# Kernel tuning notes

Hardware: AMD Instinct MI355X
Metric: run time of the kernel (lower is better)

## Reference

```python
import jax, jax.numpy as jnp
import numpy as np

INPUT_DIM = 10
SIG_DEPTH = 3
HIDDEN = 64
D_AUG = INPUT_DIM + 1  # time augmentation
LOGSIG_DIM = min(sum(D_AUG ** k // max(1, k) for k in range(1, SIG_DEPTH + 1)), 512)  # = 512
B, N = 1024, 256


def _compute_logsigs(features):
    """Vectorized computation of the per-step prefix-path signature features.

    For prefix length k+1 the torch code time-augments with linspace(0,1,k+1),
    i.e. dt = 1/k, which makes the time-related signature terms k-dependent.
    All terms reduce to cumulative sums over t, computed once for all k.
    Returns (B, N, LOGSIG_DIM); row k=0 is zeros (torch uses zeros at k=0).
    """
    Bsz, n, D = features.shape
    d = D + 1  # augmented dim (time first)
    dtype = features.dtype
    x0 = features[:, :1, :]
    inc = features[:, 1:, :] - features[:, :-1, :]          # (B, n-1, D) feature increments
    rel = features - x0                                      # x_t - x_0, (B, n, D)
    t_idx = jnp.arange(n - 1, dtype=dtype)
    # A[k-1] = sum_{t<k} t * dx_t   (time-row of level-2 term, before dt scaling)
    A = jnp.cumsum(t_idx[None, :, None] * inc, axis=1)       # (B, n-1, D)
    # Bc[k-1] = sum_{t=0}^{k-1} (x_t - x_0)   (time-column, before dt scaling)
    Bc = jnp.cumsum(rel[:, :-1, :], axis=1)                  # (B, n-1, D)
    # C[k-1] = sum_{t<k} (x_t - x_0) outer dx_t  (feature-feature level-2 block)
    C = jnp.cumsum(rel[:, :-1, :, None] * inc[:, :, None, :], axis=1)  # (B, n-1, D, D)
    ks = jnp.arange(1, n, dtype=dtype)                       # k = 1..n-1
    inv_k = 1.0 / ks
    tt = 0.5 * (ks - 1) * inv_k                              # sum t*dt^2 = (k-1)/(2k)
    # level-1: [T=1, x_k - x_0]
    sig1 = jnp.concatenate([jnp.ones((Bsz, n - 1, 1), dtype), rel[:, 1:, :]], axis=-1)  # (B, n-1, d)
    # level-2 matrix, augmented order [time, features]
    sig2 = jnp.zeros((Bsz, n - 1, d, d), dtype)
    sig2 = sig2.at[:, :, 0, 0].set(tt[None, :])
    sig2 = sig2.at[:, :, 0, 1:].set(inv_k[None, :, None] * A)
    sig2 = sig2.at[:, :, 1:, 0].set(inv_k[None, :, None] * Bc)
    sig2 = sig2.at[:, :, 1:, 1:].set(C)
    sig2f = sig2.reshape(Bsz, n - 1, d * d)
    # level-3 (torch: flatten(sig1 outer sig2_flat), truncated); only build needed rows
    sig3_len = LOGSIG_DIM - d - d * d                        # 512 - 11 - 121 = 380
    rows = (sig3_len + d * d - 1) // (d * d)                 # 4 rows of sig1 suffice
    sig3 = (sig1[..., :rows, None] * sig2f[..., None, :]).reshape(Bsz, n - 1, rows * d * d)[..., :sig3_len]
    logsig = jnp.concatenate([sig1, sig2f, sig3], axis=-1)[..., :LOGSIG_DIM]  # (B, n-1, 512)
    return jnp.concatenate([jnp.zeros((Bsz, 1, LOGSIG_DIM), dtype), logsig], axis=1)


def setup_inputs() -> dict:
    key = jax.random.key(0)
    k0, k1, k2, k3 = jax.random.split(key, 4)
    features = jax.random.normal(k0, (B, N, INPUT_DIM), jnp.float32)
    in_dim = LOGSIG_DIM + INPUT_DIM + 1  # 523
    W1 = jax.random.normal(k1, (in_dim, HIDDEN), jnp.float32) / np.sqrt(in_dim)
    b1 = jnp.zeros((HIDDEN,), jnp.float32)
    W2 = jax.random.normal(k2, (HIDDEN, HIDDEN), jnp.float32) / np.sqrt(HIDDEN)
    b2 = jnp.zeros((HIDDEN,), jnp.float32)
    W3 = jax.random.normal(k3, (HIDDEN, 1), jnp.float32) / np.sqrt(HIDDEN)
    b3 = jnp.zeros((1,), jnp.float32)
    return {"features": features, "W1": W1, "b1": b1, "W2": W2, "b2": b2, "W3": W3, "b3": b3}


def reference(features, W1, b1, W2, b2, W3, b3):
    logsigs = _compute_logsigs(features)  # (B, N, LOGSIG_DIM)
    Bsz = features.shape[0]

    def step(prev_delta, inputs):
        ls, ft = inputs  # (B, L), (B, D)
        x = jnp.concatenate([ls, ft, prev_delta], axis=-1)
        h = jax.nn.relu(x @ W1 + b1)
        h = jax.nn.relu(h @ W2 + b2)
        delta = h @ W3 + b3  # (B, 1)
        return delta, delta[:, 0]

    ls_t = jnp.swapaxes(logsigs, 0, 1)   # (N, B, L)
    ft_t = jnp.swapaxes(features, 0, 1)  # (N, B, D)
    _, deltas = jax.lax.scan(step, jnp.zeros((Bsz, 1), features.dtype), (ls_t, ft_t))
    return jnp.swapaxes(deltas, 0, 1)    # (B, N)
```

## Files before the change

### kernel.cpp

```cpp
#include <hip/hip_runtime.h>

#define NB 1024
#define NT 256
#define IND 10
#define HID 64

#define KSTEPS 14
#define XS 456
#define WMF_HALVES (KSTEPS * 4 * 64 * 8)

typedef short bf16x8 __attribute__((ext_vector_type(8)));
typedef float f32x4 __attribute__((ext_vector_type(4)));

__device__ __forceinline__ int qmap(int kk) {
    if (kk < 10) return 1 + kk;
    if (kk < 20) return 11 * (kk - 10 + 1);
    int i = (kk - 20) / 10, c = (kk - 20) % 10;
    return 11 * (i + 1) + 1 + c;
}

__device__ __forceinline__ unsigned bf16rne(float x) {
    unsigned u = __float_as_uint(x);
    return (u + 0x7fffu + ((u >> 16) & 1u)) >> 16;
}
__device__ __forceinline__ unsigned pk2(float a, float b) {
    return bf16rne(a) | (bf16rne(b) << 16);
}

__device__ float wm_value(int kk, int j, const float* __restrict__ W1,
                          const float* __restrict__ b1) {
    if (kk < 384) {
        int sec = kk >> 7;
        int rem = kk & 127;
        int w = rem >> 5, i = rem & 31;
        if (i >= 30) return 0.f;
        int q = qmap(30 * w + i);
        if (sec == 0) return W1[(11 + q) * 64 + j] + W1[(132 + q) * 64 + j];
        if (sec == 1) return W1[(253 + q) * 64 + j];
        return W1[(374 + q) * 64 + j];
    }
    if (kk < 400) {
        int i = kk - 384;
        if (i < 10) return W1[(496 + i) * 64 + j];
        if (i == 10) return W1[506 * 64 + j];
        return W1[(507 + (i - 11)) * 64 + j];
    }
    if (kk < 410) return W1[(1 + (kk - 400)) * 64 + j];
    if (kk < 420) return W1[(512 + (kk - 410)) * 64 + j];
    if (kk == 420) return W1[11 * 64 + j] + W1[132 * 64 + j];
    if (kk == 421) return W1[253 * 64 + j];
    if (kk == 422) return W1[374 * 64 + j];
    if (kk == 423) return W1[495 * 64 + j];
    if (kk == 424) return W1[0 * 64 + j];
    if (kk == 425) return b1[j];
    return 0.f;
}

__global__ void pack_mfma_kernel(const float* __restrict__ W1,
                                 const float* __restrict__ b1,
                                 unsigned short* __restrict__ Wmf) {
    int idx = blockIdx.x * 256 + threadIdx.x;
    if (idx >= WMF_HALVES) return;
    int half = idx & 7;
    int lane = (idx >> 3) & 63;
    int rec = idx >> 9;
    int s = rec >> 2, jb = rec & 3;
    int kk = 32 * s + (lane >> 4) * 8 + half;
    int j = 16 * jb + (lane & 15);
    Wmf[idx] = (unsigned short)bf16rne(wm_value(kk, j, W1, b1));
}

__global__ __launch_bounds__(256, 1) void presig9_kernel(
    const float* __restrict__ features, const unsigned short* __restrict__ Wmf,
    float* __restrict__ pre1) {
    const int b = blockIdx.x;
    const int tid = threadIdx.x;
    const int l = tid & 63;
    const int wu = tid >> 6;

    __shared__ __align__(16) float sF[NT * IND];
    __shared__ __align__(16) unsigned short sX[64 * XS];
    __shared__ float sBase[128];

    {
        const float4* src = (const float4*)(features + b * (NT * IND));
        float4* dst = (float4*)sF;
        for (int e = tid; e < NT * IND / 4; e += 256) dst[e] = src[e];
    }
    float f0[IND];
#pragma unroll
    for (int c = 0; c < IND; ++c) f0[c] = features[b * (NT * IND) + c];

    if (tid < 128) sBase[tid] = 0.f;
    __syncthreads();

    for (int tile = 0; tile < 4; ++tile) {
        const int t0 = tile * 64;

        const int r = t0 + l;
        float rf = (float)r;
        float fr[IND], rel[IND], inc[IND];
#pragma unroll
        for (int c = 0; c < IND; ++c) fr[c] = sF[r * IND + c];
#pragma unroll
        for (int c = 0; c < IND; ++c) rel[c] = fr[c] - f0[c];
        {
            bool last = (r >= NT - 1);
#pragma unroll
            for (int c = 0; c < IND; ++c)
                inc[c] = last ? 0.f : (sF[(r + 1) * IND + c] - fr[c]);
        }
        float p[30], own[30];
        if (wu == 0) {
#pragma unroll
            for (int c = 0; c < 10; ++c) p[c] = rf * inc[c];
#pragma unroll
            for (int i = 0; i < 10; ++i) p[10 + i] = rel[i];
#pragma unroll
            for (int c = 0; c < 10; ++c) p[20 + c] = rel[0] * inc[c];
        } else {
            const int i0 = 3 * wu - 2;
#pragma unroll
            for (int q = 0; q < 30; ++q) {
                int i = i0 + q / 10, c = q % 10;
                p[q] = rel[i] * inc[c];
            }
        }
#pragma unroll
        for (int i = 0; i < 30; ++i) own[i] = p[i];
#pragma unroll
        for (int dsh = 0; dsh < 6; ++dsh) {
            const int d = 1 << dsh;
            bool ok = (l >= d);
#pragma unroll
            for (int i = 0; i < 30; ++i) {
                float v = __shfl_up(p[i], d, 64);
                if (ok) p[i] += v;
            }
        }
        float inv_r = (r > 0) ? 1.f / rf : 0.f;
        float v[30];
#pragma unroll
        for (int i = 0; i < 30; ++i) {
            float x = sBase[wu * 32 + i] + p[i] - own[i];
            if (wu == 0 && i < 20) x *= inv_r;
            v[i] = x;
        }

        {
            float g0 = rel[0], g1 = rel[1];
            uint4* xr = (uint4*)&sX[l * XS];
            uint4* x0 = (uint4*)&sX[l * XS + 128];
            uint4* x1 = (uint4*)&sX[l * XS + 256];
#pragma unroll
            for (int q = 0; q < 3; ++q) {
                uint4 tr, t0v, t1v;
                tr.x = pk2(v[8*q+0], v[8*q+1]); tr.y = pk2(v[8*q+2], v[8*q+3]);
                tr.z = pk2(v[8*q+4], v[8*q+5]); tr.w = pk2(v[8*q+6], v[8*q+7]);
                t0v.x = pk2(g0*v[8*q+0], g0*v[8*q+1]); t0v.y = pk2(g0*v[8*q+2], g0*v[8*q+3]);
                t0v.z = pk2(g0*v[8*q+4], g0*v[8*q+5]); t0v.w = pk2(g0*v[8*q+6], g0*v[8*q+7]);
                t1v.x = pk2(g1*v[8*q+0], g1*v[8*q+1]); t1v.y = pk2(g1*v[8*q+2], g1*v[8*q+3]);
                t1v.z = pk2(g1*v[8*q+4], g1*v[8*q+5]); t1v.w = pk2(g1*v[8*q+6], g1*v[8*q+7]);
                xr[wu * 4 + q] = tr; x0[wu * 4 + q] = t0v; x1[wu * 4 + q] = t1v;
            }
            {
                uint4 tr, t0v, t1v;
                tr.x = pk2(v[24], v[25]); tr.y = pk2(v[26], v[27]);
                tr.z = pk2(v[28], v[29]); tr.w = 0u;
                t0v.x = pk2(g0*v[24], g0*v[25]); t0v.y = pk2(g0*v[26], g0*v[27]);
                t0v.z = pk2(g0*v[28], g0*v[29]); t0v.w = 0u;
                t1v.x = pk2(g1*v[24], g1*v[25]); t1v.y = pk2(g1*v[26], g1*v[27]);
                t1v.z = pk2(g1*v[28], g1*v[29]); t1v.w = 0u;
                xr[wu * 4 + 3] = tr; x0[wu * 4 + 3] = t0v; x1[wu * 4 + 3] = t1v;
            }
        }
        if (wu == 0) {
            float g2 = rel[2];
            float ttv = 0.5f * (rf - 1.f) * inv_r;
            float gate = (r > 0) ? 1.f : 0.f;
            uint4* xe = (uint4*)&sX[l * XS + 384];
            uint4 u;
            u.x = pk2(g2*v[0], g2*v[1]);  u.y = pk2(g2*v[2], g2*v[3]);
            u.z = pk2(g2*v[4], g2*v[5]);  u.w = pk2(g2*v[6], g2*v[7]);
            xe[0] = u;
            u.x = pk2(g2*v[8], g2*v[9]);  u.y = pk2(g2*v[10], g2*v[20]);
            u.z = pk2(g2*v[21], g2*v[22]); u.w = pk2(g2*v[23], g2*v[24]);
            xe[1] = u;
            u.x = pk2(rel[0], rel[1]); u.y = pk2(rel[2], rel[3]);
            u.z = pk2(rel[4], rel[5]); u.w = pk2(rel[6], rel[7]);
            xe[2] = u;
            u.x = pk2(rel[8], rel[9]); u.y = pk2(fr[0], fr[1]);
            u.z = pk2(fr[2], fr[3]);   u.w = pk2(fr[4], fr[5]);
            xe[3] = u;
            u.x = pk2(fr[6], fr[7]); u.y = pk2(fr[8], fr[9]);
            u.z = pk2(ttv, ttv * rel[0]); u.w = pk2(ttv * rel[1], ttv * rel[2]);
            xe[4] = u;
            u.x = pk2(gate, 1.0f); u.y = 0u; u.z = 0u; u.w = 0u;
            xe[5] = u;
            u.x = 0u; u.y = 0u; u.z = 0u; u.w = 0u;
            xe[6] = u; xe[7] = u;
        }
        if (l == 63) {
#pragma unroll
            for (int i = 0; i < 30; ++i) sBase[wu * 32 + i] += p[i];
        }
        __syncthreads();

        {
            const int m = l & 15, quad = l >> 4;
            const unsigned short* arow = &sX[(16 * wu + m) * XS + 8 * quad];
            const bf16x8* bp = (const bf16x8*)Wmf;
            f32x4 ac0 = {0.f, 0.f, 0.f, 0.f}, ac1 = ac0, ac2 = ac0, ac3 = ac0;
#pragma unroll
            for (int s = 0; s < KSTEPS; ++s) {
                bf16x8 af = *(const bf16x8*)(arow + 32 * s);
                bf16x8 bf0 = bp[(s * 4 + 0) * 64 + l];
                bf16x8 bf1 = bp[(s * 4 + 1) * 64 + l];
                bf16x8 bf2 = bp[(s * 4 + 2) * 64 + l];
                bf16x8 bf3 = bp[(s * 4 + 3) * 64 + l];
                ac0 = __builtin_amdgcn_mfma_f32_16x16x32_bf16(af, bf0, ac0, 0, 0, 0);
                ac1 = __builtin_amdgcn_mfma_f32_16x16x32_bf16(af, bf1, ac1, 0, 0, 0);
                ac2 = __builtin_amdgcn_mfma_f32_16x16x32_bf16(af, bf2, ac2, 0, 0, 0);
                ac3 = __builtin_amdgcn_mfma_f32_16x16x32_bf16(af, bf3, ac3, 0, 0, 0);
            }
            float* op = pre1 + b * (NT * HID) + (t0 + 16 * wu) * HID + m;
            const int rowb = quad * 4;
#pragma unroll
            for (int reg = 0; reg < 4; ++reg) {
                op[(rowb + reg) * HID + 0]  = ac0[reg];
                op[(rowb + reg) * HID + 16] = ac1[reg];
                op[(rowb + reg) * HID + 32] = ac2[reg];
                op[(rowb + reg) * HID + 48] = ac3[reg];
            }
        }
        __syncthreads();
    }
}

template <int CTRL, int RMASK>
__device__ __forceinline__ float dpp_add(float x) {
    int v = __builtin_amdgcn_update_dpp(0, __float_as_int(x), CTRL, RMASK, 0xf, false);
    return x + __int_as_float(v);
}

__device__ __forceinline__ float rl(float x, int lane) {
    return __uint_as_float(__builtin_amdgcn_readlane(__float_as_uint(x), lane));
}

__global__ __launch_bounds__(64, 1) void scan6_kernel(
    const float* __restrict__ pre1, const float* __restrict__ W1,
    const float* __restrict__ W2, const float* __restrict__ b2,
    const float* __restrict__ W3, const float* __restrict__ b3,
    float* __restrict__ out) {
    const int b = blockIdx.x;
    const int l = threadIdx.x;
    const int m = l & 15, q = l >> 4;

#define BUILD_B(dst, ks, nb) { \
        const int k0 = 32 * (ks) + 8 * q; \
        const int n = 16 * (nb) + m; \
        float x0 = W2[(k0 + 0) * 64 + n], x1 = W2[(k0 + 1) * 64 + n]; \
        float x2 = W2[(k0 + 2) * 64 + n], x3 = W2[(k0 + 3) * 64 + n]; \
        float x4 = W2[(k0 + 4) * 64 + n], x5 = W2[(k0 + 5) * 64 + n]; \
        float x6 = W2[(k0 + 6) * 64 + n], x7 = W2[(k0 + 7) * 64 + n]; \
        unsigned u0, u1, u2, u3; \
        asm("v_cvt_pk_bf16_f32 %0, %1, %2" : "=v"(u0) : "v"(x0), "v"(x1)); \
        asm("v_cvt_pk_bf16_f32 %0, %1, %2" : "=v"(u1) : "v"(x2), "v"(x3)); \
        asm("v_cvt_pk_bf16_f32 %0, %1, %2" : "=v"(u2) : "v"(x4), "v"(x5)); \
        asm("v_cvt_pk_bf16_f32 %0, %1, %2" : "=v"(u3) : "v"(x6), "v"(x7)); \
        union { unsigned uu[4]; bf16x8 v; } cv; \
        cv.uu[0] = u0; cv.uu[1] = u1; cv.uu[2] = u2; cv.uu[3] = u3; \
        dst = cv.v; }

    bf16x8 Bf0, Bf1, Bf2, Bf3, Bf4, Bf5, Bf6, Bf7;
    BUILD_B(Bf0, 0, 0) BUILD_B(Bf1, 0, 1) BUILD_B(Bf2, 0, 2) BUILD_B(Bf3, 0, 3)
    BUILD_B(Bf4, 1, 0) BUILD_B(Bf5, 1, 1) BUILD_B(Bf6, 1, 2) BUILD_B(Bf7, 1, 3)
#undef BUILD_B

    float w1a[8], w1b[8];
#pragma unroll
    for (int i = 0; i < 8; ++i) {
        w1a[i] = W1[522 * 64 + 8 * q + i];
        w1b[i] = W1[522 * 64 + 32 + 8 * q + i];
    }
    float b2s0 = b2[m],      b2s1 = b2[16 + m],
          b2s2 = b2[32 + m], b2s3 = b2[48 + m];
    float w3s0 = W3[m] * 0.25f,      w3s1 = W3[16 + m] * 0.25f,
          w3s2 = W3[32 + m] * 0.25f, w3s3 = W3[48 + m] * 0.25f;
    float b3v = b3[0];

    const float* pb_ = pre1 + b * (NT * HID);
    const int o1 = 8 * q, o2 = 8 * q + 4, o3 = 32 + 8 * q, o4 = 36 + 8 * q;
    float delta = 0.f;
    float outbuf = 0.f;

#define STEP6(pa, pb, pc, pd, mm) { \
        float hA0 = fmaxf(fmaf(delta, w1a[0], (pa).x), 0.f); \
        float hA1 = fmaxf(fmaf(delta, w1a[1], (pa).y), 0.f); \
        float hA2 = fmaxf(fmaf(delta, w1a[2], (pa).z), 0.f); \
        float hA3 = fmaxf(fmaf(delta, w1a[3], (pa).w), 0.f); \
        float hA4 = fmaxf(fmaf(delta, w1a[4], (pb).x), 0.f); \
        float hA5 = fmaxf(fmaf(delta, w1a[5], (pb).y), 0.f); \
        float hA6 = fmaxf(fmaf(delta, w1a[6], (pb).z), 0.f); \
        float hA7 = fmaxf(fmaf(delta, w1a[7], (pb).w), 0.f); \
        float hB0 = fmaxf(fmaf(delta, w1b[0], (pc).x), 0.f); \
        float hB1 = fmaxf(fmaf(delta, w1b[1], (pc).y), 0.f); \
        float hB2 = fmaxf(fmaf(delta, w1b[2], (pc).z), 0.f); \
        float hB3 = fmaxf(fmaf(delta, w1b[3], (pc).w), 0.f); \
        float hB4 = fmaxf(fmaf(delta, w1b[4], (pd).x), 0.f); \
        float hB5 = fmaxf(fmaf(delta, w1b[5], (pd).y), 0.f); \
        float hB6 = fmaxf(fmaf(delta, w1b[6], (pd).z), 0.f); \
        float hB7 = fmaxf(fmaf(delta, w1b[7], (pd).w), 0.f); \
        unsigned uA0, uA1, uA2, uA3, uB0, uB1, uB2, uB3; \
        asm("v_cvt_pk_bf16_f32 %0, %1, %2" : "=v"(uA0) : "v"(hA0), "v"(hA1)); \
        asm("v_cvt_pk_bf16_f32 %0, %1, %2" : "=v"(uA1) : "v"(hA2), "v"(hA3)); \
        asm("v_cvt_pk_bf16_f32 %0, %1, %2" : "=v"(uA2) : "v"(hA4), "v"(hA5)); \
        asm("v_cvt_pk_bf16_f32 %0, %1, %2" : "=v"(uA3) : "v"(hA6), "v"(hA7)); \
        asm("v_cvt_pk_bf16_f32 %0, %1, %2" : "=v"(uB0) : "v"(hB0), "v"(hB1)); \
        asm("v_cvt_pk_bf16_f32 %0, %1, %2" : "=v"(uB1) : "v"(hB2), "v"(hB3)); \
        asm("v_cvt_pk_bf16_f32 %0, %1, %2" : "=v"(uB2) : "v"(hB4), "v"(hB5)); \
        asm("v_cvt_pk_bf16_f32 %0, %1, %2" : "=v"(uB3) : "v"(hB6), "v"(hB7)); \
        union { unsigned uu[4]; bf16x8 v; } cA, cB; \
        cA.uu[0] = uA0; cA.uu[1] = uA1; cA.uu[2] = uA2; cA.uu[3] = uA3; \
        cB.uu[0] = uB0; cB.uu[1] = uB1; cB.uu[2] = uB2; cB.uu[3] = uB3; \
        f32x4 z = {0.f, 0.f, 0.f, 0.f}; \
        f32x4 c0 = __builtin_amdgcn_mfma_f32_16x16x32_bf16(cA.v, Bf0, z, 0, 0, 0); \
        f32x4 c1 = __builtin_amdgcn_mfma_f32_16x16x32_bf16(cA.v, Bf1, z, 0, 0, 0); \
        f32x4 c2 = __builtin_amdgcn_mfma_f32_16x16x32_bf16(cA.v, Bf2, z, 0, 0, 0); \
        f32x4 c3 = __builtin_amdgcn_mfma_f32_16x16x32_bf16(cA.v, Bf3, z, 0, 0, 0); \
        c0 = __builtin_amdgcn_mfma_f32_16x16x32_bf16(cB.v, Bf4, c0, 0, 0, 0); \
        c1 = __builtin_amdgcn_mfma_f32_16x16x32_bf16(cB.v, Bf5, c1, 0, 0, 0); \
        c2 = __builtin_amdgcn_mfma_f32_16x16x32_bf16(cB.v, Bf6, c2, 0, 0, 0); \
        c3 = __builtin_amdgcn_mfma_f32_16x16x32_bf16(cB.v, Bf7, c3, 0, 0, 0); \
        float qv; \
        qv =      fmaxf(c0[0] + b2s0, 0.f) * w3s0; \
        qv = fmaf(fmaxf(c1[0] + b2s1, 0.f), w3s1, qv); \
        qv = fmaf(fmaxf(c2[0] + b2s2, 0.f), w3s2, qv); \
        qv = fmaf(fmaxf(c3[0] + b2s3, 0.f), w3s3, qv); \
        qv = dpp_add<0x111, 0xf>(qv); \
        qv = dpp_add<0x112, 0xf>(qv); \
        qv = dpp_add<0x114, 0xf>(qv); \
        qv = dpp_add<0x118, 0xf>(qv); \
        qv = dpp_add<0x142, 0xa>(qv); \
        qv = dpp_add<0x143, 0xc>(qv); \
        delta = rl(qv, 63) + b3v; \
        if (l == ((mm) & 63)) outbuf = delta; \
        if (((mm) & 63) == 63) out[b * NT + ((mm) & ~63) + l] = outbuf; }

    float4 s0a, s0b, s0c, s0d, s1a, s1b, s1c, s1d,
           s2a, s2b, s2c, s2d, s3a, s3b, s3c, s3d;
    float4 t0a, t0b, t0c, t0d, t1a, t1b, t1c, t1d,
           t2a, t2b, t2c, t2d, t3a, t3b, t3c, t3d;
#define LD(dsta, dstb, dstc, dstd, tt) { \
        const float* base = &pb_[(tt) * 64]; \
        dsta = *(const float4*)&base[o1]; dstb = *(const float4*)&base[o2]; \
        dstc = *(const float4*)&base[o3]; dstd = *(const float4*)&base[o4]; }

    LD(s0a, s0b, s0c, s0d, 0) LD(s1a, s1b, s1c, s1d, 1)
    LD(s2a, s2b, s2c, s2d, 2) LD(s3a, s3b, s3c, s3d, 3)
    LD(t0a, t0b, t0c, t0d, 4) LD(t1a, t1b, t1c, t1d, 5)
    LD(t2a, t2b, t2c, t2d, 6) LD(t3a, t3b, t3c, t3d, 7)

    for (int g = 0; g < NT; g += 8) {
        STEP6(s0a, s0b, s0c, s0d, g + 0)
        STEP6(s1a, s1b, s1c, s1d, g + 1)
        STEP6(s2a, s2b, s2c, s2d, g + 2)
        STEP6(s3a, s3b, s3c, s3d, g + 3)
        LD(s0a, s0b, s0c, s0d, min(g + 8,  NT - 1))
        LD(s1a, s1b, s1c, s1d, min(g + 9,  NT - 1))
        LD(s2a, s2b, s2c, s2d, min(g + 10, NT - 1))
        LD(s3a, s3b, s3c, s3d, min(g + 11, NT - 1))
        STEP6(t0a, t0b, t0c, t0d, g + 4)
        STEP6(t1a, t1b, t1c, t1d, g + 5)
        STEP6(t2a, t2b, t2c, t2d, g + 6)
        STEP6(t3a, t3b, t3c, t3d, g + 7)
        LD(t0a, t0b, t0c, t0d, min(g + 12, NT - 1))
        LD(t1a, t1b, t1c, t1d, min(g + 13, NT - 1))
        LD(t2a, t2b, t2c, t2d, min(g + 14, NT - 1))
        LD(t3a, t3b, t3c, t3d, min(g + 15, NT - 1))
    }
#undef LD
#undef STEP6
}

__global__ __launch_bounds__(256) void logsig_hedge_fallback(
    const float* __restrict__ features, const float* __restrict__ W1,
    const float* __restrict__ b1, const float* __restrict__ W2,
    const float* __restrict__ b2, const float* __restrict__ W3,
    const float* __restrict__ b3, float* __restrict__ out) {
    const int b = blockIdx.x;
    const int tid = threadIdx.x;
    const int j = tid & 63;
    const int s = tid >> 6;

    __shared__ __align__(16) float sF[NT * IND];
    __shared__ __align__(16) float sSig[128];
    __shared__ float sA[IND], sB[IND], sC[IND * IND];
    __shared__ float sRel[IND];
    __shared__ __align__(16) float sPart[4 * 64];
    __shared__ __align__(16) float sH1[64];

    for (int idx = tid; idx < NT * IND; idx += 256)
        sF[idx] = features[b * (NT * IND) + idx];
    if (tid < 100) sC[tid] = 0.f;
    else if (tid < 110) sA[tid - 100] = 0.f;
    else if (tid < 120) sB[tid - 110] = 0.f;
    else if (tid >= 121 && tid < 128) sSig[tid] = 0.f;

    float vs[32], vb[32], vc[32];
#pragma unroll
    for (int mm = 0; mm < 32; ++mm) {
        int mp = 32 * s + mm;
        if (mp < 121) {
            vs[mm] = W1[(11 + mp) * 64 + j] + W1[(132 + mp) * 64 + j];
            vb[mm] = W1[(253 + mp) * 64 + j];
            vc[mm] = W1[(374 + mp) * 64 + j];
        } else { vs[mm] = 0.f; vb[mm] = 0.f; vc[mm] = 0.f; }
    }
    float ex[17];
#pragma unroll
    for (int q = 0; q < 17; ++q) ex[q] = 0.f;
    if (s == 1) {
#pragma unroll
        for (int q = 0; q < 11; ++q) ex[q] = W1[q * 64 + j];
    } else if (s == 2) {
#pragma unroll
        for (int q = 0; q < 10; ++q) ex[q] = W1[(512 + q) * 64 + j];
        ex[10] = b1[j];
    } else if (s == 3) {
#pragma unroll
        for (int q = 0; q < 17; ++q) ex[q] = W1[(495 + q) * 64 + j];
    }
    float w2p[16];
#pragma unroll
    for (int ii = 0; ii < 16; ++ii) w2p[ii] = W2[(16 * s + ii) * 64 + j];

    float w1l = 0.f, b2j = 0.f, w3j = 0.f, b3v = 0.f;
    if (s == 0) { w1l = W1[522 * 64 + j]; b2j = b2[j]; w3j = W3[j]; b3v = b3[0]; }
    float delta = 0.f;

    __syncthreads();

    for (int m = 0; m < NT; ++m) {
        if (m > 0) {
            if (tid < 100) {
                int i = tid / 10, c = tid % 10;
                float rp = sF[(m - 1) * 10 + i] - sF[i];
                float ic = sF[m * 10 + c] - sF[(m - 1) * 10 + c];
                sC[tid] += rp * ic;
            } else if (tid < 110) {
                int i = tid - 100;
                sA[i] += (float)(m - 1) * (sF[m * 10 + i] - sF[(m - 1) * 10 + i]);
            } else if (tid < 120) {
                int i = tid - 110;
                sB[i] += sF[(m - 1) * 10 + i] - sF[i];
            }
            __syncthreads();
            float inv_k = 1.0f / (float)m;
            if (tid == 0) sSig[0] = 0.5f * (float)(m - 1) * inv_k;
            else if (tid < 11) sSig[tid] = inv_k * sA[tid - 1];
            else if (tid < 121) {
                int i = tid / 11 - 1, c = tid % 11;
                sSig[tid] = (c == 0) ? inv_k * sB[i] : sC[i * 10 + (c - 1)];
            } else if (tid < 131) {
                int f = tid - 121;
                sRel[f] = sF[m * 10 + f] - sF[f];
            }
            __syncthreads();
        }
        float part = 0.f;
        if (m > 0) {
            float pa = 0.f, pb = 0.f, pc = 0.f;
#pragma unroll
            for (int q = 0; q < 8; ++q) {
                float4 sv = *(const float4*)&sSig[32 * s + 4 * q];
                pa = fmaf(sv.x, vs[4 * q + 0], pa);
                pb = fmaf(sv.x, vb[4 * q + 0], pb);
                pc = fmaf(sv.x, vc[4 * q + 0], pc);
                pa = fmaf(sv.y, vs[4 * q + 1], pa);
                pb = fmaf(sv.y, vb[4 * q + 1], pb);
                pc = fmaf(sv.y, vc[4 * q + 1], pc);
                pa = fmaf(sv.z, vs[4 * q + 2], pa);
                pb = fmaf(sv.z, vb[4 * q + 2], pb);
                pc = fmaf(sv.z, vc[4 * q + 2], pc);
                pa = fmaf(sv.w, vs[4 * q + 3], pa);
                pb = fmaf(sv.w, vb[4 * q + 3], pb);
                pc = fmaf(sv.w, vc[4 * q + 3], pc);
            }
            part = pa + sRel[0] * pb + sRel[1] * pc;
            if (s == 3) {
                float pd = 0.f;
#pragma unroll
                for (int q = 0; q < 17; ++q) pd = fmaf(sSig[q], ex[q], pd);
                part = fmaf(sRel[2], pd, part);
            }
            if (s == 1) {
                part += ex[0];
#pragma unroll
                for (int i = 0; i < 10; ++i) part = fmaf(sRel[i], ex[1 + i], part);
            }
        }
        if (s == 2) {
            float pf = ex[10];
#pragma unroll
            for (int f = 0; f < 10; ++f) pf = fmaf(sF[m * 10 + f], ex[f], pf);
            part += pf;
        }
        sPart[s * 64 + j] = part;
        __syncthreads();
        if (s == 0) {
            float x = sPart[j] + sPart[64 + j] + sPart[128 + j] + sPart[192 + j];
            sH1[j] = fmaxf(fmaf(delta, w1l, x), 0.f);
        }
        __syncthreads();
        {
            float hp = 0.f;
#pragma unroll
            for (int q = 0; q < 4; ++q) {
                float4 hv = *(const float4*)&sH1[16 * s + 4 * q];
                hp = fmaf(hv.x, w2p[4 * q + 0], hp);
                hp = fmaf(hv.y, w2p[4 * q + 1], hp);
                hp = fmaf(hv.z, w2p[4 * q + 2], hp);
                hp = fmaf(hv.w, w2p[4 * q + 3], hp);
            }
            sPart[s * 64 + j] = hp;
        }
        __syncthreads();
        if (s == 0) {
            float x2 = sPart[j] + sPart[64 + j] + sPart[128 + j] + sPart[192 + j] + b2j;
            float h2 = fmaxf(x2, 0.f);
            float dv = h2 * w3j;
#pragma unroll
            for (int off = 32; off > 0; off >>= 1) dv += __shfl_xor(dv, off, 64);
            delta = dv + b3v;
            if (j == 0) out[b * NT + m] = delta;
        }
        __syncthreads();
    }
}

extern "C" void kernel_launch(void* const* d_in, const int* in_sizes, int n_in,
                              void* d_out, int out_size, void* d_ws, size_t ws_size,
                              hipStream_t stream) {
    const float* features = (const float*)d_in[0];
    const float* W1 = (const float*)d_in[1];
    const float* b1 = (const float*)d_in[2];
    const float* W2 = (const float*)d_in[3];
    const float* b2 = (const float*)d_in[4];
    const float* W3 = (const float*)d_in[5];
    const float* b3 = (const float*)d_in[6];
    float* out = (float*)d_out;

    const size_t wmf_bytes = (size_t)WMF_HALVES * 2;
    const size_t w_pad     = ((wmf_bytes + 255) / 256) * 256;
    const size_t pre_bytes = (size_t)NB * NT * HID * sizeof(float);
    if (ws_size >= w_pad + pre_bytes) {
        unsigned short* Wmf = (unsigned short*)d_ws;
        float* pre1 = (float*)((char*)d_ws + w_pad);
        pack_mfma_kernel<<<(WMF_HALVES + 255) / 256, 256, 0, stream>>>(W1, b1, Wmf);
        presig9_kernel<<<NB, 256, 0, stream>>>(features, Wmf, pre1);
        scan6_kernel<<<NB, 64, 0, stream>>>(pre1, W1, W2, b2, W3, b3, out);
    } else {
        logsig_hedge_fallback<<<NB, 256, 0, stream>>>(features, W1, b1, W2, b2, W3, b3, out);
    }
}
```

Measured before the change: 266.4 us.

## Stream scan inputs through LDS via async global_load_lds with ring buffer

Replaces the register double-buffered global loads in the sequential scan kernel with direct global-to-LDS async loads into a 16-step ring buffer, prefetching three 4-step chunks ahead and reading the next step from LDS while computing the current one. It also splits the two chained MFMA accumulations into independent pairs summed afterward, which shortens the serial dependency per step. Constants are pinned in VGPRs. This is meant to cut latency on the critical serial path, at the cost of extra LDS traffic and a hand-managed vmcnt wait whose correctness depends on load ordering.

```diff
diff --git a/kernel.cpp b/kernel.cpp
--- a/kernel.cpp
+++ b/kernel.cpp
@@ -247,7 +247,13 @@
     return __uint_as_float(__builtin_amdgcn_readlane(__float_as_uint(x), lane));
 }
 
-__global__ __launch_bounds__(64, 1) void scan6_kernel(
+__device__ __forceinline__ void gload_lds16(const float* g, float* l) {
+    __builtin_amdgcn_global_load_lds(
+        (const __attribute__((address_space(1))) void*)g,
+        (__attribute__((address_space(3))) void*)l, 16, 0, 0);
+}
+
+__global__ __launch_bounds__(64, 1) void scan7_kernel(
     const float* __restrict__ pre1, const float* __restrict__ W1,
     const float* __restrict__ W2, const float* __restrict__ b2,
     const float* __restrict__ W3, const float* __restrict__ b3,
@@ -255,6 +261,8 @@
     const int b = blockIdx.x;
     const int l = threadIdx.x;
     const int m = l & 15, q = l >> 4;
+
+    __shared__ __align__(1024) float sP[16][64];
 
 #define BUILD_B(dst, ks, nb) { \
         const int k0 = 32 * (ks) + 8 * q; \
@@ -288,13 +296,31 @@
     float w3s0 = W3[m] * 0.25f,      w3s1 = W3[16 + m] * 0.25f,
           w3s2 = W3[32 + m] * 0.25f, w3s3 = W3[48 + m] * 0.25f;
     float b3v = b3[0];
+#define PIN4(a, b_, c_, d_) asm volatile("" : "+v"(a), "+v"(b_), "+v"(c_), "+v"(d_));
+    PIN4(w1a[0], w1a[1], w1a[2], w1a[3]) PIN4(w1a[4], w1a[5], w1a[6], w1a[7])
+    PIN4(w1b[0], w1b[1], w1b[2], w1b[3]) PIN4(w1b[4], w1b[5], w1b[6], w1b[7])
+    PIN4(b2s0, b2s1, b2s2, b2s3) PIN4(w3s0, w3s1, w3s2, w3s3)
+    asm volatile("" : "+v"(b3v));
+#undef PIN4
 
     const float* pb_ = pre1 + b * (NT * HID);
-    const int o1 = 8 * q, o2 = 8 * q + 4, o3 = 32 + 8 * q, o4 = 36 + 8 * q;
     float delta = 0.f;
     float outbuf = 0.f;
 
-#define STEP6(pa, pb, pc, pd, mm) { \
+#define ISSUE_G(cc) { \
+        int ci_ = (cc); \
+        gload_lds16(pb_ + ci_ * 256 + 4 * l, &sP[4 * (ci_ & 3)][0]); }
+
+#define DSRD(da, db, dc, dd, stepi) { \
+        const char* base_ = (const char*)&sP[0][0] + \
+            ((((stepi) & 15) * 256) + q * 32); \
+        da = *(const float4*)(base_); \
+        db = *(const float4*)(base_ + 16); \
+        dc = *(const float4*)(base_ + 128); \
+        dd = *(const float4*)(base_ + 144); }
+
+#define STEP7(pa, pb, pc, pd, na, nb_, nc_, nd_, nstep, mm) { \
+        DSRD(na, nb_, nc_, nd_, nstep) \
         float hA0 = fmaxf(fmaf(delta, w1a[0], (pa).x), 0.f); \
         float hA1 = fmaxf(fmaf(delta, w1a[1], (pa).y), 0.f); \
         float hA2 = fmaxf(fmaf(delta, w1a[2], (pa).z), 0.f); \
@@ -325,18 +351,22 @@
         cB.uu[0] = uB0; cB.uu[1] = uB1; cB.uu[2] = uB2; cB.uu[3] = uB3; \
         f32x4 z = {0.f, 0.f, 0.f, 0.f}; \
         f32x4 c0 = __builtin_amdgcn_mfma_f32_16x16x32_bf16(cA.v, Bf0, z, 0, 0, 0); \
+        f32x4 d0 = __builtin_amdgcn_mfma_f32_16x16x32_bf16(cB.v, Bf4, z, 0, 0, 0); \
         f32x4 c1 = __builtin_amdgcn_mfma_f32_16x16x32_bf16(cA.v, Bf1, z, 0, 0, 0); \
+        f32x4 d1 = __builtin_amdgcn_mfma_f32_16x16x32_bf16(cB.v, Bf5, z, 0, 0, 0); \
         f32x4 c2 = __builtin_amdgcn_mfma_f32_16x16x32_bf16(cA.v, Bf2, z, 0, 0, 0); \
+        f32x4 d2 = __builtin_amdgcn_mfma_f32_16x16x32_bf16(cB.v, Bf6, z, 0, 0, 0); \
         f32x4 c3 = __builtin_amdgcn_mfma_f32_16x16x32_bf16(cA.v, Bf3, z, 0, 0, 0); \
-        c0 = __builtin_amdgcn_mfma_f32_16x16x32_bf16(cB.v, Bf4, c0, 0, 0, 0); \
-        c1 = __builtin_amdgcn_mfma_f32_16x16x32_bf16(cB.v, Bf5, c1, 0, 0, 0); \
-        c2 = __builtin_amdgcn_mfma_f32_16x16x32_bf16(cB.v, Bf6, c2, 0, 0, 0); \
-        c3 = __builtin_amdgcn_mfma_f32_16x16x32_bf16(cB.v, Bf7, c3, 0, 0, 0); \
-        float qv; \
-        qv =      fmaxf(c0[0] + b2s0, 0.f) * w3s0; \
-        qv = fmaf(fmaxf(c1[0] + b2s1, 0.f), w3s1, qv); \
-        qv = fmaf(fmaxf(c2[0] + b2s2, 0.f), w3s2, qv); \
-        qv = fmaf(fmaxf(c3[0] + b2s3, 0.f), w3s3, qv); \
+        f32x4 d3 = __builtin_amdgcn_mfma_f32_16x16x32_bf16(cB.v, Bf7, z, 0, 0, 0); \
+        float v0 = c0[0] + d0[0]; \
+        float v1 = c1[0] + d1[0]; \
+        float v2 = c2[0] + d2[0]; \
+        float v3 = c3[0] + d3[0]; \
+        float e0 = fmaxf(v0 + b2s0, 0.f) * w3s0; \
+        float e1 = fmaxf(v1 + b2s1, 0.f) * w3s1; \
+        float e2 = fmaxf(v2 + b2s2, 0.f) * w3s2; \
+        float e3 = fmaxf(v3 + b2s3, 0.f) * w3s3; \
+        float qv = (e0 + e1) + (e2 + e3); \
         qv = dpp_add<0x111, 0xf>(qv); \
         qv = dpp_add<0x112, 0xf>(qv); \
         qv = dpp_add<0x114, 0xf>(qv); \
@@ -347,40 +377,24 @@
         if (l == ((mm) & 63)) outbuf = delta; \
         if (((mm) & 63) == 63) out[b * NT + ((mm) & ~63) + l] = outbuf; }
 
-    float4 s0a, s0b, s0c, s0d, s1a, s1b, s1c, s1d,
-           s2a, s2b, s2c, s2d, s3a, s3b, s3c, s3d;
-    float4 t0a, t0b, t0c, t0d, t1a, t1b, t1c, t1d,
-           t2a, t2b, t2c, t2d, t3a, t3b, t3c, t3d;
-#define LD(dsta, dstb, dstc, dstd, tt) { \
-        const float* base = &pb_[(tt) * 64]; \
-        dsta = *(const float4*)&base[o1]; dstb = *(const float4*)&base[o2]; \
-        dstc = *(const float4*)&base[o3]; dstd = *(const float4*)&base[o4]; }
-
-    LD(s0a, s0b, s0c, s0d, 0) LD(s1a, s1b, s1c, s1d, 1)
-    LD(s2a, s2b, s2c, s2d, 2) LD(s3a, s3b, s3c, s3d, 3)
-    LD(t0a, t0b, t0c, t0d, 4) LD(t1a, t1b, t1c, t1d, 5)
-    LD(t2a, t2b, t2c, t2d, 6) LD(t3a, t3b, t3c, t3d, 7)
-
-    for (int g = 0; g < NT; g += 8) {
-        STEP6(s0a, s0b, s0c, s0d, g + 0)
-        STEP6(s1a, s1b, s1c, s1d, g + 1)
-        STEP6(s2a, s2b, s2c, s2d, g + 2)
-        STEP6(s3a, s3b, s3c, s3d, g + 3)
-        LD(s0a, s0b, s0c, s0d, min(g + 8,  NT - 1))
-        LD(s1a, s1b, s1c, s1d, min(g + 9,  NT - 1))
-        LD(s2a, s2b, s2c, s2d, min(g + 10, NT - 1))
-        LD(s3a, s3b, s3c, s3d, min(g + 11, NT - 1))
-        STEP6(t0a, t0b, t0c, t0d, g + 4)
-        STEP6(t1a, t1b, t1c, t1d, g + 5)
-        STEP6(t2a, t2b, t2c, t2d, g + 6)
-        STEP6(t3a, t3b, t3c, t3d, g + 7)
-        LD(t0a, t0b, t0c, t0d, min(g + 12, NT - 1))
-        LD(t1a, t1b, t1c, t1d, min(g + 13, NT - 1))
-        LD(t2a, t2b, t2c, t2d, min(g + 14, NT - 1))
-        LD(t3a, t3b, t3c, t3d, min(g + 15, NT - 1))
-    }
-#undef LD
-#undef STEP6
+    ISSUE_G(0); ISSUE_G(1); ISSUE_G(2);
+    asm volatile("s_waitcnt vmcnt(2)" ::: "memory");
+
+    float4 Aa, Ab, Ac, Ad, Ba, Bb, Bc, Bd;
+    DSRD(Aa, Ab, Ac, Ad, 0)
+
+    for (int c = 0; c < 64; ++c) {
+        ISSUE_G(min(c + 3, 63));
+        asm volatile("s_waitcnt vmcnt(2)" ::: "memory");
+        const int g = 4 * c;
+        STEP7(Aa, Ab, Ac, Ad, Ba, Bb, Bc, Bd, g + 1, g + 0)
+        STEP7(Ba, Bb, Bc, Bd, Aa, Ab, Ac, Ad, g + 2, g + 1)
+        STEP7(Aa, Ab, Ac, Ad, Ba, Bb, Bc, Bd, g + 3, g + 2)
+        STEP7(Ba, Bb, Bc, Bd, Aa, Ab, Ac, Ad, g + 4, g + 3)
+    }
+#undef STEP7
+#undef DSRD
+#undef ISSUE_G
 }
 
 __global__ __launch_bounds__(256) void logsig_hedge_fallback(
@@ -559,7 +573,7 @@
         float* pre1 = (float*)((char*)d_ws + w_pad);
         pack_mfma_kernel<<<(WMF_HALVES + 255) / 256, 256, 0, stream>>>(W1, b1, Wmf);
         presig9_kernel<<<NB, 256, 0, stream>>>(features, Wmf, pre1);
-        scan6_kernel<<<NB, 64, 0, stream>>>(pre1, W1, W2, b2, W3, b3, out);
+        scan7_kernel<<<NB, 64, 0, stream>>>(pre1, W1, W2, b2, W3, b3, out);
     } else {
         logsig_hedge_fallback<<<NB, 256, 0, stream>>>(features, W1, b1, W2, b2, W3, b3, out);
     }
```

Result: slower. 276.0 us (+3.6%).
